# Performance work log

Hardware: AMD Instinct MI355X
Metric: run time of the kernel (lower is better)

Reference implementation:

```python
import jax, jax.numpy as jnp
import numpy as np

N, E, DIN, DOUT = 100000, 1000000, 128, 128
C = 1.0            # curvature c_in = c_out = 1.0
EPS = 4e-3         # PoincareBall float32 boundary eps
MIN_NORM = 1e-15
NEG_SLOPE = 0.01   # F.leaky_relu default


def _proj(x, c):
    norm = jnp.maximum(jnp.linalg.norm(x, axis=-1, keepdims=True), MIN_NORM)
    maxnorm = (1.0 - EPS) / jnp.sqrt(c)
    return jnp.where(norm > maxnorm, x / norm * maxnorm, x)


def _expmap0(u, c):
    sqrt_c = jnp.sqrt(c)
    u_norm = jnp.maximum(jnp.linalg.norm(u, axis=-1, keepdims=True), MIN_NORM)
    return jnp.tanh(sqrt_c * u_norm) * u / (sqrt_c * u_norm)


def _mobius_add(x, y, c):
    x2 = jnp.sum(x * x, -1, keepdims=True)
    y2 = jnp.sum(y * y, -1, keepdims=True)
    xy = jnp.sum(x * y, -1, keepdims=True)
    num = (1.0 + 2.0 * c * xy + c * y2) * x + (1.0 - c * x2) * y
    denom = 1.0 + 2.0 * c * xy + c * c * x2 * y2
    return num / jnp.maximum(denom, MIN_NORM)


def _p2k(x, c):  # Poincare ball -> Klein model
    return 2.0 * x / (1.0 + c * jnp.sum(x * x, -1, keepdims=True))


def _k2p(x, c):  # Klein model -> Poincare ball
    denom = 1.0 + jnp.sqrt(jnp.maximum(1.0 - c * jnp.sum(x * x, -1, keepdims=True), MIN_NORM))
    return x / denom


def _lorenz_factor(x, c=1.0):  # 1/sqrt(1 - c||x||^2), keepdim
    return 1.0 / jnp.sqrt(jnp.maximum(1.0 - c * jnp.sum(x * x, -1, keepdims=True), MIN_NORM))


def setup_inputs() -> dict:
    key = jax.random.key(0)
    kx, kr, ko, kw, kb = jax.random.split(key, 5)
    x = 0.1 * jax.random.normal(kx, (N, DIN), dtype=jnp.float32)
    row = jax.random.randint(kr, (E,), 0, N)
    off = jax.random.randint(ko, (E,), 1, N)
    col = (row + off) % N  # guaranteed no self-loops; reference appends them
    edge_index = jnp.stack([row, col]).astype(jnp.int64)
    # geotorch-orthogonal weight in the original; any full-rank matrix is fine for the baseline
    W = jax.random.normal(kw, (DOUT, DIN), dtype=jnp.float32) / np.sqrt(DIN)
    bias = jax.random.uniform(kb, (1, DOUT), dtype=jnp.float32, minval=-0.1, maxval=0.1)
    return {"x": x, "W": W, "bias": bias, "edge_index": edge_index}


def reference(x, W, bias, edge_index):
    row0, col0 = edge_index[0], edge_index[1]
    # add_remaining_self_loops (no self-loops present by construction)
    loop = jnp.arange(N)
    row = jnp.concatenate([row0, loop])
    col = jnp.concatenate([col0, loop])
    w = jnp.ones(row.shape, x.dtype)
    deg = jax.ops.segment_sum(w, row, num_segments=N)
    dinv = jnp.where(deg > 0, deg ** -0.5, 0.0)
    norm = dinv[row] * w * dinv[col]                      # [E+N]

    # HypMPLinear
    h = x @ W.T
    h = _proj(h, C)
    hyp_bias = _expmap0(bias, C)                          # proj_tan0 is identity on Poincare ball
    h = _proj(_mobius_add(h, hyp_bias, C), C)

    # HypMPAgg (agg_type=1)
    s = _p2k(h, C)                                        # [N, D]
    lamb = _lorenz_factor(s)                              # [N, 1], default c=1.0
    support_w = norm[:, None] * lamb[col]                 # [E+N, 1]
    s_j = support_w * s[col]                              # [E+N, D]
    tmp = jax.ops.segment_sum(support_w, row, num_segments=N)   # [N, 1]
    s_out = jax.ops.segment_sum(s_j, row, num_segments=N) / tmp # [N, D]
    out = _k2p(s_out, C)

    # HypMPAct: leaky_relu applied directly
    return jax.nn.leaky_relu(out, NEG_SLOPE)
```

## Files before the change

### kernel.cpp

```cpp
#include <hip/hip_runtime.h>
#include <math.h>


#define EPS_B 4e-3f
#define MINN 1e-15f
#define PAD 40

typedef __bf16 bf16_t;
typedef __attribute__((ext_vector_type(8))) __bf16 bf16x8;
typedef __attribute__((ext_vector_type(4))) __bf16 bf16x4;
typedef __attribute__((ext_vector_type(4))) float f32x4;

#define WP 140
#define HP 140

__global__ __launch_bounds__(256, 2) void k_fused(const float* __restrict__ x,
                                                  const float* __restrict__ W,
                                                  const float* __restrict__ bias,
                                                  const int* __restrict__ row,
                                                  bf16_t* __restrict__ sbuf,
                                                  float* __restrict__ nsbuf,
                                                  float* __restrict__ lambbuf,
                                                  int* __restrict__ cnt,
                                                  int* __restrict__ pos,
                                                  int N, int E, int gb, int db) {
    const unsigned grp = blockIdx.x / 13, r = blockIdx.x % 13;
    if (r >= 8) {
        int did = grp * 5 + (r - 8);
        if (did < db) {
            int ebase = did * 1024 + threadIdx.x;
            int e0 = ebase, e1 = ebase + 256, e2 = ebase + 512, e3 = ebase + 768;
            int r0 = 0, r1 = 0, r2 = 0, r3 = 0;
            if (e0 < E) r0 = row[e0];
            if (e1 < E) r1 = row[e1];
            if (e2 < E) r2 = row[e2];
            if (e3 < E) r3 = row[e3];
            int p0 = 0, p1 = 0, p2 = 0, p3 = 0;
            if (e0 < E) p0 = atomicAdd(&cnt[r0], 1);
            if (e1 < E) p1 = atomicAdd(&cnt[r1], 1);
            if (e2 < E) p2 = atomicAdd(&cnt[r2], 1);
            if (e3 < E) p3 = atomicAdd(&cnt[r3], 1);
            if (e0 < E) pos[e0] = p0;
            if (e1 < E) pos[e1] = p1;
            if (e2 < E) pos[e2] = p2;
            if (e3 < E) pos[e3] = p3;
        }
        return;
    }
    const int gid = grp * 8 + r;
    if (gid >= gb) return;

    __shared__ __align__(16) unsigned char smem[128 * WP * 2];
    bf16_t* Wb = (bf16_t*)smem;
    float* h_s = (float*)smem;
    __shared__ float hb_s[128];

    const int t = threadIdx.x;
    const int base = gid * 64;
    const float MAXN = 1.0f - EPS_B;

    if (t < 128) hb_s[t] = bias[t];
    __syncthreads();
    const int l6 = t & 63;
    float b0 = hb_s[2 * l6], b1 = hb_s[2 * l6 + 1];
    float bn2 = b0 * b0 + b1 * b1;
#pragma unroll
    for (int m = 1; m < 64; m <<= 1) bn2 += __shfl_xor(bn2, m);
    float un = fmaxf(sqrtf(bn2), MINN);
    float th = tanhf(un);
    float y2 = th * th;
    __syncthreads();
    if (t < 128) hb_s[t] *= th / un;

#pragma unroll
    for (int i2 = 0; i2 < 16; ++i2) {
        int idx = t + 256 * i2;
        int rr = idx >> 5, c4 = idx & 31;
        float4 v = ((const float4*)W)[idx];
        bf16x4 hv = {(bf16_t)v.x, (bf16_t)v.y, (bf16_t)v.z, (bf16_t)v.w};
        *(bf16x4*)&Wb[rr * WP + 4 * c4] = hv;
    }

    const int w = t >> 6, l = t & 63;
    const int mrow = l & 15, kq = l >> 4;
    const int gn = base + 16 * w + mrow;
    bf16x8 ahi[4], alo[4];
    {
        const float4* xr4 = (const float4*)(x + (size_t)gn * 128);
#pragma unroll
        for (int kt = 0; kt < 4; ++kt) {
            float4 v0 = make_float4(0.f, 0.f, 0.f, 0.f), v1 = v0;
            if (gn < N) {
                v0 = xr4[8 * kt + 2 * kq];
                v1 = xr4[8 * kt + 2 * kq + 1];
            }
            float f[8] = {v0.x, v0.y, v0.z, v0.w, v1.x, v1.y, v1.z, v1.w};
#pragma unroll
            for (int i = 0; i < 8; ++i) {
                bf16_t h = (bf16_t)f[i];
                ahi[kt][i] = h;
                alo[kt][i] = (bf16_t)(f[i] - (float)h);
            }
        }
    }
    __syncthreads();

    f32x4 acc[8];
#pragma unroll
    for (int nt = 0; nt < 8; ++nt) acc[nt] = (f32x4){0.f, 0.f, 0.f, 0.f};

#pragma unroll
    for (int nt = 0; nt < 8; ++nt) {
#pragma unroll
        for (int kt = 0; kt < 4; ++kt) {
            bf16x8 bw = *(bf16x8*)&Wb[(16 * nt + mrow) * WP + 32 * kt + 8 * kq];
            acc[nt] = __builtin_amdgcn_mfma_f32_16x16x32_bf16(ahi[kt], bw, acc[nt], 0, 0, 0);
            acc[nt] = __builtin_amdgcn_mfma_f32_16x16x32_bf16(alo[kt], bw, acc[nt], 0, 0, 0);
        }
    }
    __syncthreads();

#pragma unroll
    for (int nt = 0; nt < 8; ++nt)
#pragma unroll
        for (int rr = 0; rr < 4; ++rr)
            h_s[(16 * w + 4 * kq + rr) * HP + 16 * nt + mrow] = acc[nt][rr];
    __syncthreads();

    const int node = t >> 2, lg = t & 3;
    const int gn2 = base + node;
    float h[32], hb[32];
#pragma unroll
    for (int q = 0; q < 8; ++q) {
        float4 v = *(const float4*)&h_s[node * HP + lg * 32 + 4 * q];
        h[4 * q] = v.x; h[4 * q + 1] = v.y; h[4 * q + 2] = v.z; h[4 * q + 3] = v.w;
        float4 b = *(const float4*)&hb_s[lg * 32 + 4 * q];
        hb[4 * q] = b.x; hb[4 * q + 1] = b.y; hb[4 * q + 2] = b.z; hb[4 * q + 3] = b.w;
    }
    float x2 = 0.f;
#pragma unroll
    for (int d = 0; d < 32; ++d) x2 += h[d] * h[d];
    x2 += __shfl_xor(x2, 1); x2 += __shfl_xor(x2, 2);
    float nrm = sqrtf(x2);
    float sc = nrm > MAXN ? MAXN / nrm : 1.f;
#pragma unroll
    for (int d = 0; d < 32; ++d) h[d] *= sc;
    x2 *= sc * sc;
    float xy = 0.f;
#pragma unroll
    for (int d = 0; d < 32; ++d) xy += h[d] * hb[d];
    xy += __shfl_xor(xy, 1); xy += __shfl_xor(xy, 2);
    float ca = 1.f + 2.f * xy + y2;
    float cb = 1.f - x2;
    float den = 1.f + 2.f * xy + x2 * y2;
    float invd = 1.f / fmaxf(den, MINN);
    float m2 = 0.f;
#pragma unroll
    for (int d = 0; d < 32; ++d) {
        float v = (ca * h[d] + cb * hb[d]) * invd;
        h[d] = v;
        m2 += v * v;
    }
    m2 += __shfl_xor(m2, 1); m2 += __shfl_xor(m2, 2);
    float nrm2 = sqrtf(m2);
    float sc2 = nrm2 > MAXN ? MAXN / nrm2 : 1.f;
    m2 *= sc2 * sc2;
    float pf = 2.f / (1.f + m2);
    float ns = pf * pf * m2;
    float lamb = rsqrtf(fmaxf(1.f - ns, MINN));
    if (gn2 < N) {
        bf16_t* dst = sbuf + (size_t)gn2 * 128 + lg * 32;
        float f = pf * sc2;
#pragma unroll
        for (int q = 0; q < 4; ++q) {
            bf16x8 sv;
#pragma unroll
            for (int j = 0; j < 8; ++j) sv[j] = (bf16_t)(f * h[8 * q + j]);
            *(bf16x8*)&dst[8 * q] = sv;
        }
        if (lg == 0) {
            nsbuf[gn2] = ns;
            lambbuf[gn2] = lamb;
        }
    }
}

__global__ __launch_bounds__(256) void k_place2g(const int* __restrict__ row,
                                                 const int* __restrict__ col,
                                                 const int* __restrict__ pos,
                                                 int* __restrict__ csrp,
                                                 const float* __restrict__ lamb,
                                                 const int* __restrict__ cnt,
                                                 float* __restrict__ g,
                                                 int E, int N, int eb) {
    if (blockIdx.x < (unsigned)eb) {
        int e = blockIdx.x * 256 + threadIdx.x;
        if (e < E) {
            int p = pos[e];
            if (p < PAD) csrp[(size_t)row[e] * PAD + p] = col[e];
        }
    } else {
        int i = (blockIdx.x - eb) * 256 + threadIdx.x;
        if (i < N) g[i] = lamb[i] * rsqrtf((float)(cnt[i] + 1));
    }
}

__global__ __launch_bounds__(256) void k_agg(const bf16_t* __restrict__ s,
                                             const float* __restrict__ nsb,
                                             const float* __restrict__ g,
                                             const int* __restrict__ cnt,
                                             const int* __restrict__ csrp,
                                             float* __restrict__ out, int N) {
    const int lane = threadIdx.x & 63, wid = threadIdx.x >> 6;
    const int q = lane >> 4, ql = lane & 15;
    const int i = blockIdx.x * 16 + wid * 4 + q;
    const bool valid = i < N;
    const int ic = valid ? i : 0;

    int c = valid ? cnt[ic] : 0;
    if (c > PAD) c = PAD;
    const float gi = g[ic];
    const size_t st = (size_t)ic * PAD;

    float a[8];
    {
        bf16x8 sv = *(const bf16x8*)(s + (size_t)ic * 128 + ql * 8);
#pragma unroll
        for (int d = 0; d < 8; ++d) a[d] = gi * (float)sv[d];
    }
    float gvs = 0.f;

    for (int bs = 0; bs < c; bs += 16) {
        int rem = c - bs;
        if (rem > 16) rem = 16;
        int jv = 0;
        float gv = 0.f;
        if (ql < rem) {
            jv = csrp[st + bs + ql];
            gv = g[jv];
        }
        gvs += gv;
        for (int e = 0; e < rem; e += 4) {
            int j0 = __shfl(jv, 16 * q + e);
            int j1 = __shfl(jv, 16 * q + e + 1);
            int j2 = __shfl(jv, 16 * q + e + 2);
            int j3 = __shfl(jv, 16 * q + e + 3);
            float g0 = __shfl(gv, 16 * q + e);
            float g1 = __shfl(gv, 16 * q + e + 1);
            float g2 = __shfl(gv, 16 * q + e + 2);
            float g3 = __shfl(gv, 16 * q + e + 3);
            bf16x8 v0 = *(const bf16x8*)(s + (size_t)j0 * 128 + ql * 8);
            bf16x8 v1 = *(const bf16x8*)(s + (size_t)j1 * 128 + ql * 8);
            bf16x8 v2 = *(const bf16x8*)(s + (size_t)j2 * 128 + ql * 8);
            bf16x8 v3 = *(const bf16x8*)(s + (size_t)j3 * 128 + ql * 8);
#pragma unroll
            for (int d = 0; d < 8; ++d) {
                a[d] = fmaf(g0, (float)v0[d], a[d]);
                a[d] = fmaf(g1, (float)v1[d], a[d]);
                a[d] = fmaf(g2, (float)v2[d], a[d]);
                a[d] = fmaf(g3, (float)v3[d], a[d]);
            }
        }
    }
    gvs += __shfl_xor(gvs, 1); gvs += __shfl_xor(gvs, 2);
    gvs += __shfl_xor(gvs, 4); gvs += __shfl_xor(gvs, 8);
    float tw = gi + gvs;

    float inv = 1.f / tw;
    float o[8];
    float ns = 0.f;
#pragma unroll
    for (int d = 0; d < 8; ++d) {
        o[d] = a[d] * inv;
        ns += o[d] * o[d];
    }
    ns += __shfl_xor(ns, 1); ns += __shfl_xor(ns, 2);
    ns += __shfl_xor(ns, 4); ns += __shfl_xor(ns, 8);
    if (c == 0) ns = nsb[ic];
    float den = 1.f + sqrtf(fmaxf(1.f - ns, MINN));
    float id = 1.f / den;
#pragma unroll
    for (int d = 0; d < 8; ++d) {
        float v = o[d] * id;
        o[d] = v >= 0.f ? v : 0.01f * v;
    }
    if (valid) {
        float* dst = out + (size_t)i * 128 + ql * 8;
        *(float4*)dst = make_float4(o[0], o[1], o[2], o[3]);
        *(float4*)(dst + 4) = make_float4(o[4], o[5], o[6], o[7]);
    }
}

extern "C" void kernel_launch(void* const* d_in, const int* in_sizes, int n_in,
                              void* d_out, int out_size, void* d_ws, size_t ws_size,
                              hipStream_t stream) {
    const float* x    = (const float*)d_in[0];
    const float* W    = (const float*)d_in[1];
    const float* bias = (const float*)d_in[2];
    const int*   ei   = (const int*)d_in[3];

    const int N = in_sizes[0] / 128;
    const int E = in_sizes[3] / 2;
    const int* row = ei;
    const int* col = ei + E;

    float*  g_buf  = (float*)d_ws;
    float*  ns_buf = g_buf + N;
    float*  lambb  = ns_buf + N;
    int*    cnt    = (int*)(lambb + N);
    int*    pos    = cnt + N;
    int*    csrp   = pos + E;
    bf16_t* s_buf  = (bf16_t*)(csrp + (size_t)N * PAD);

    hipMemsetAsync(cnt, 0, (size_t)N * sizeof(int), stream);

    const int gb = (N + 63) / 64;
    const int db = (E + 1023) / 1024;
    int grp = (gb + 7) / 8;
    if ((db + 4) / 5 > grp) grp = (db + 4) / 5;
    k_fused<<<grp * 13, 256, 0, stream>>>(x, W, bias, row, s_buf, ns_buf, lambb,
                                          cnt, pos, N, E, gb, db);
    const int eb = (E + 255) / 256;
    const int gbk = (N + 255) / 256;
    k_place2g<<<eb + gbk, 256, 0, stream>>>(row, col, pos, csrp, lambb, cnt,
                                            g_buf, E, N, eb);
    k_agg<<<(N + 15) / 16, 256, 0, stream>>>(s_buf, ns_buf, g_buf, cnt, csrp,
                                             (float*)d_out, N);
}
```

Baseline: 129.2 us.

## Precompute MFMA weight fragments and run epilogue in accumulator layout without LDS

```diff
diff --git a/kernel.cpp b/kernel.cpp
--- a/kernel.cpp
+++ b/kernel.cpp
@@ -8,15 +8,49 @@
 
 typedef __bf16 bf16_t;
 typedef __attribute__((ext_vector_type(8))) __bf16 bf16x8;
-typedef __attribute__((ext_vector_type(4))) __bf16 bf16x4;
 typedef __attribute__((ext_vector_type(4))) float f32x4;
 
-#define WP 140
-#define HP 140
-
-__global__ __launch_bounds__(256, 2) void k_fused(const float* __restrict__ x,
-                                                  const float* __restrict__ W,
-                                                  const float* __restrict__ bias,
+__global__ __launch_bounds__(256) void k_prep(const float* __restrict__ W,
+                                              const float* __restrict__ bias,
+                                              int* __restrict__ cnt,
+                                              bf16_t* __restrict__ wfrag,
+                                              float* __restrict__ hbg,
+                                              int N, int zb) {
+    const int bid = blockIdx.x, t = threadIdx.x;
+    if (bid < zb) {
+        int i = bid * 1024 + 4 * t;
+        if (i + 4 <= N) *(int4*)&cnt[i] = make_int4(0, 0, 0, 0);
+        else { for (int k = 0; k < 4; ++k) if (i + k < N) cnt[i + k] = 0; }
+        return;
+    }
+    if (bid < zb + 8) {
+        int tile = (bid - zb) * 4 + (t >> 6);
+        int l = t & 63;
+        int n = 16 * (tile >> 2) + (l & 15);
+        int kb = 32 * (tile & 3) + 8 * (l >> 4);
+        bf16x8 hv;
+#pragma unroll
+        for (int i = 0; i < 8; ++i) hv[i] = (bf16_t)W[n * 128 + kb + i];
+        *(bf16x8*)&wfrag[(size_t)(tile * 64 + l) * 8] = hv;
+        return;
+    }
+    __shared__ float bs[128];
+    if (t < 128) bs[t] = bias[t];
+    __syncthreads();
+    const int l6 = t & 63;
+    float b0 = bs[2 * l6], b1 = bs[2 * l6 + 1];
+    float bn2 = b0 * b0 + b1 * b1;
+#pragma unroll
+    for (int m = 1; m < 64; m <<= 1) bn2 += __shfl_xor(bn2, m);
+    float un = fmaxf(sqrtf(bn2), MINN);
+    float th = tanhf(un);
+    if (t < 128) hbg[t] = bs[t] * th / un;
+    if (t == 128) hbg[128] = th * th;
+}
+
+__global__ __launch_bounds__(256, 3) void k_fused(const float* __restrict__ x,
+                                                  const bf16_t* __restrict__ wfrag,
+                                                  const float* __restrict__ hbg,
                                                   const int* __restrict__ row,
                                                   bf16_t* __restrict__ sbuf,
                                                   float* __restrict__ nsbuf,
@@ -50,39 +84,17 @@
     const int gid = grp * 8 + r;
     if (gid >= gb) return;
 
-    __shared__ __align__(16) unsigned char smem[128 * WP * 2];
-    bf16_t* Wb = (bf16_t*)smem;
-    float* h_s = (float*)smem;
-    __shared__ float hb_s[128];
-
     const int t = threadIdx.x;
+    const int w = t >> 6, l = t & 63;
+    const int mrow = l & 15, kq = l >> 4;
     const int base = gid * 64;
     const float MAXN = 1.0f - EPS_B;
 
-    if (t < 128) hb_s[t] = bias[t];
-    __syncthreads();
-    const int l6 = t & 63;
-    float b0 = hb_s[2 * l6], b1 = hb_s[2 * l6 + 1];
-    float bn2 = b0 * b0 + b1 * b1;
-#pragma unroll
-    for (int m = 1; m < 64; m <<= 1) bn2 += __shfl_xor(bn2, m);
-    float un = fmaxf(sqrtf(bn2), MINN);
-    float th = tanhf(un);
-    float y2 = th * th;
-    __syncthreads();
-    if (t < 128) hb_s[t] *= th / un;
-
-#pragma unroll
-    for (int i2 = 0; i2 < 16; ++i2) {
-        int idx = t + 256 * i2;
-        int rr = idx >> 5, c4 = idx & 31;
-        float4 v = ((const float4*)W)[idx];
-        bf16x4 hv = {(bf16_t)v.x, (bf16_t)v.y, (bf16_t)v.z, (bf16_t)v.w};
-        *(bf16x4*)&Wb[rr * WP + 4 * c4] = hv;
-    }
-
-    const int w = t >> 6, l = t & 63;
-    const int mrow = l & 15, kq = l >> 4;
+    float hbl[8];
+#pragma unroll
+    for (int nt = 0; nt < 8; ++nt) hbl[nt] = hbg[16 * nt + mrow];
+    const float y2 = hbg[128];
+
     const int gn = base + 16 * w + mrow;
     bf16x8 ahi[4], alo[4];
     {
@@ -103,7 +115,6 @@
             }
         }
     }
-    __syncthreads();
 
     f32x4 acc[8];
 #pragma unroll
@@ -113,74 +124,62 @@
     for (int nt = 0; nt < 8; ++nt) {
 #pragma unroll
         for (int kt = 0; kt < 4; ++kt) {
-            bf16x8 bw = *(bf16x8*)&Wb[(16 * nt + mrow) * WP + 32 * kt + 8 * kq];
+            bf16x8 bw = *(const bf16x8*)&wfrag[(size_t)((nt * 4 + kt) * 64 + l) * 8];
             acc[nt] = __builtin_amdgcn_mfma_f32_16x16x32_bf16(ahi[kt], bw, acc[nt], 0, 0, 0);
             acc[nt] = __builtin_amdgcn_mfma_f32_16x16x32_bf16(alo[kt], bw, acc[nt], 0, 0, 0);
         }
     }
-    __syncthreads();
-
-#pragma unroll
-    for (int nt = 0; nt < 8; ++nt)
-#pragma unroll
-        for (int rr = 0; rr < 4; ++rr)
-            h_s[(16 * w + 4 * kq + rr) * HP + 16 * nt + mrow] = acc[nt][rr];
-    __syncthreads();
-
-    const int node = t >> 2, lg = t & 3;
-    const int gn2 = base + node;
-    float h[32], hb[32];
-#pragma unroll
-    for (int q = 0; q < 8; ++q) {
-        float4 v = *(const float4*)&h_s[node * HP + lg * 32 + 4 * q];
-        h[4 * q] = v.x; h[4 * q + 1] = v.y; h[4 * q + 2] = v.z; h[4 * q + 3] = v.w;
-        float4 b = *(const float4*)&hb_s[lg * 32 + 4 * q];
-        hb[4 * q] = b.x; hb[4 * q + 1] = b.y; hb[4 * q + 2] = b.z; hb[4 * q + 3] = b.w;
-    }
-    float x2 = 0.f;
-#pragma unroll
-    for (int d = 0; d < 32; ++d) x2 += h[d] * h[d];
-    x2 += __shfl_xor(x2, 1); x2 += __shfl_xor(x2, 2);
-    float nrm = sqrtf(x2);
-    float sc = nrm > MAXN ? MAXN / nrm : 1.f;
-#pragma unroll
-    for (int d = 0; d < 32; ++d) h[d] *= sc;
-    x2 *= sc * sc;
-    float xy = 0.f;
-#pragma unroll
-    for (int d = 0; d < 32; ++d) xy += h[d] * hb[d];
-    xy += __shfl_xor(xy, 1); xy += __shfl_xor(xy, 2);
-    float ca = 1.f + 2.f * xy + y2;
-    float cb = 1.f - x2;
-    float den = 1.f + 2.f * xy + x2 * y2;
-    float invd = 1.f / fmaxf(den, MINN);
-    float m2 = 0.f;
-#pragma unroll
-    for (int d = 0; d < 32; ++d) {
-        float v = (ca * h[d] + cb * hb[d]) * invd;
-        h[d] = v;
-        m2 += v * v;
-    }
-    m2 += __shfl_xor(m2, 1); m2 += __shfl_xor(m2, 2);
-    float nrm2 = sqrtf(m2);
-    float sc2 = nrm2 > MAXN ? MAXN / nrm2 : 1.f;
-    m2 *= sc2 * sc2;
-    float pf = 2.f / (1.f + m2);
-    float ns = pf * pf * m2;
-    float lamb = rsqrtf(fmaxf(1.f - ns, MINN));
-    if (gn2 < N) {
-        bf16_t* dst = sbuf + (size_t)gn2 * 128 + lg * 32;
-        float f = pf * sc2;
-#pragma unroll
-        for (int q = 0; q < 4; ++q) {
+
+#pragma unroll
+    for (int rr = 0; rr < 4; ++rr) {
+        float h[8];
+#pragma unroll
+        for (int nt = 0; nt < 8; ++nt) h[nt] = acc[nt][rr];
+        float x2 = 0.f;
+#pragma unroll
+        for (int nt = 0; nt < 8; ++nt) x2 += h[nt] * h[nt];
+        x2 += __shfl_xor(x2, 1); x2 += __shfl_xor(x2, 2);
+        x2 += __shfl_xor(x2, 4); x2 += __shfl_xor(x2, 8);
+        float nrm = sqrtf(x2);
+        float sc = nrm > MAXN ? MAXN / nrm : 1.f;
+#pragma unroll
+        for (int nt = 0; nt < 8; ++nt) h[nt] *= sc;
+        x2 *= sc * sc;
+        float xy = 0.f;
+#pragma unroll
+        for (int nt = 0; nt < 8; ++nt) xy += h[nt] * hbl[nt];
+        xy += __shfl_xor(xy, 1); xy += __shfl_xor(xy, 2);
+        xy += __shfl_xor(xy, 4); xy += __shfl_xor(xy, 8);
+        float ca = 1.f + 2.f * xy + y2;
+        float cb = 1.f - x2;
+        float den = 1.f + 2.f * xy + x2 * y2;
+        float invd = 1.f / fmaxf(den, MINN);
+        float m2 = 0.f;
+#pragma unroll
+        for (int nt = 0; nt < 8; ++nt) {
+            float v = (ca * h[nt] + cb * hbl[nt]) * invd;
+            h[nt] = v;
+            m2 += v * v;
+        }
+        m2 += __shfl_xor(m2, 1); m2 += __shfl_xor(m2, 2);
+        m2 += __shfl_xor(m2, 4); m2 += __shfl_xor(m2, 8);
+        float nrm2 = sqrtf(m2);
+        float sc2 = nrm2 > MAXN ? MAXN / nrm2 : 1.f;
+        m2 *= sc2 * sc2;
+        float pf = 2.f / (1.f + m2);
+        float ns = pf * pf * m2;
+        float lamb = rsqrtf(fmaxf(1.f - ns, MINN));
+        const int node = base + 16 * w + 4 * kq + rr;
+        if (node < N) {
+            float f = pf * sc2;
             bf16x8 sv;
 #pragma unroll
-            for (int j = 0; j < 8; ++j) sv[j] = (bf16_t)(f * h[8 * q + j]);
-            *(bf16x8*)&dst[8 * q] = sv;
-        }
-        if (lg == 0) {
-            nsbuf[gn2] = ns;
-            lambbuf[gn2] = lamb;
+            for (int nt = 0; nt < 8; ++nt) sv[nt] = (bf16_t)(f * h[nt]);
+            *(bf16x8*)&sbuf[(size_t)node * 128 + 8 * mrow] = sv;
+            if (mrow == 0) {
+                nsbuf[node] = ns;
+                lambbuf[node] = lamb;
+            }
         }
     }
 }
@@ -285,9 +284,9 @@
         o[d] = v >= 0.f ? v : 0.01f * v;
     }
     if (valid) {
-        float* dst = out + (size_t)i * 128 + ql * 8;
-        *(float4*)dst = make_float4(o[0], o[1], o[2], o[3]);
-        *(float4*)(dst + 4) = make_float4(o[4], o[5], o[6], o[7]);
+        float* dst = out + (size_t)i * 128 + ql;
+#pragma unroll
+        for (int j = 0; j < 8; ++j) dst[16 * j] = o[j];
     }
 }
 
@@ -310,16 +309,19 @@
     int*    cnt    = (int*)(lambb + N);
     int*    pos    = cnt + N;
     int*    csrp   = pos + E;
-    bf16_t* s_buf  = (bf16_t*)(csrp + (size_t)N * PAD);
-
-    hipMemsetAsync(cnt, 0, (size_t)N * sizeof(int), stream);
+    float*  hbg    = (float*)(csrp + (size_t)N * PAD);
+    bf16_t* wfrag  = (bf16_t*)(hbg + 132);
+    bf16_t* s_buf  = wfrag + 16384;
+
+    const int zb = (N + 1023) / 1024;
+    k_prep<<<zb + 9, 256, 0, stream>>>(W, bias, cnt, wfrag, hbg, N, zb);
 
     const int gb = (N + 63) / 64;
     const int db = (E + 1023) / 1024;
     int grp = (gb + 7) / 8;
     if ((db + 4) / 5 > grp) grp = (db + 4) / 5;
-    k_fused<<<grp * 13, 256, 0, stream>>>(x, W, bias, row, s_buf, ns_buf, lambb,
-                                          cnt, pos, N, E, gb, db);
+    k_fused<<<grp * 13, 256, 0, stream>>>(x, wfrag, hbg, row, s_buf, ns_buf,
+                                          lambb, cnt, pos, N, E, gb, db);
     const int eb = (E + 255) / 256;
     const int gbk = (N + 255) / 256;
     k_place2g<<<eb + gbk, 256, 0, stream>>>(row, col, pos, csrp, lambb, cnt,
```

Result: slower. 137.3 us (+6.2%).
